# Performance work log

Measured on AMD Instinct MI355X. Metric: run time of the kernel, lower is better.

The kernel has to match this reference:

```python
import jax, jax.numpy as jnp
import numpy as np

B, CIN, T = 16, 80, 2048
C = 768          # channels
M = 512          # n_embeddings
D = 64           # z_dim
H = 256          # c_dim
N_MLP = 4        # hidden Linear(C, C) layers
LN_EPS = 1e-5
COMMIT = 0.25


def setup_inputs() -> dict:
    key = jax.random.key(0)
    ks = jax.random.split(key, 12)
    s = 0.02
    mels = jax.random.normal(ks[0], (B, CIN, T), dtype=jnp.float32)
    conv_w = jax.random.normal(ks[1], (C, CIN, 4), dtype=jnp.float32) * s  # [out, in, k]
    ln_gamma = jnp.ones((N_MLP + 1, C), dtype=jnp.float32)
    ln_beta = jnp.zeros((N_MLP + 1, C), dtype=jnp.float32)
    w_hidden = jax.random.normal(ks[2], (N_MLP, C, C), dtype=jnp.float32) * s  # [i, out, in]
    w_out = jax.random.normal(ks[3], (D, C), dtype=jnp.float32) * s
    embedding = jax.random.uniform(ks[4], (M, D), dtype=jnp.float32,
                                   minval=-1.0 / 512, maxval=1.0 / 512)
    w_ih = jax.random.normal(ks[5], (4 * H, D), dtype=jnp.float32) * s
    w_hh = jax.random.normal(ks[6], (4 * H, H), dtype=jnp.float32) * s
    b_ih = jnp.zeros((4 * H,), dtype=jnp.float32)
    b_hh = jnp.zeros((4 * H,), dtype=jnp.float32)
    return {"mels": mels, "conv_w": conv_w, "ln_gamma": ln_gamma, "ln_beta": ln_beta,
            "w_hidden": w_hidden, "w_out": w_out, "embedding": embedding,
            "w_ih": w_ih, "w_hh": w_hh, "b_ih": b_ih, "b_hh": b_hh}


def _layer_norm(x, g, b):
    mu = jnp.mean(x, axis=-1, keepdims=True)
    var = jnp.mean(jnp.square(x - mu), axis=-1, keepdims=True)
    return (x - mu) * jax.lax.rsqrt(var + LN_EPS) * g + b


def _lstm(x, w_ih, w_hh, b_ih, b_hh):
    # x: [B, T, D] -> outputs [B, T, H]; torch gate order i, f, g, o
    xg = jnp.einsum('btd,gd->btg', x, w_ih) + b_ih + b_hh  # precompute input gates

    def step(carry, xg_t):
        h, c = carry
        gates = xg_t + h @ w_hh.T
        i, f, g, o = jnp.split(gates, 4, axis=-1)
        c = jax.nn.sigmoid(f) * c + jax.nn.sigmoid(i) * jnp.tanh(g)
        h = jax.nn.sigmoid(o) * jnp.tanh(c)
        return (h, c), h

    h0 = jnp.zeros((x.shape[0], H), dtype=x.dtype)
    (_, _), hs = jax.lax.scan(step, (h0, h0), jnp.swapaxes(xg, 0, 1))
    return jnp.swapaxes(hs, 0, 1)


def reference(mels, conv_w, ln_gamma, ln_beta, w_hidden, w_out, embedding,
              w_ih, w_hh, b_ih, b_hh):
    # Conv1d(k=4, stride=2, pad=1, no bias): [B, CIN, T] -> [B, C, T//2]
    h = jax.lax.conv_general_dilated(
        mels, conv_w, window_strides=(2,), padding=[(1, 1)],
        dimension_numbers=('NCH', 'OIH', 'NCH'))
    h = jnp.swapaxes(h, 1, 2)  # [B, T', C]

    for i in range(N_MLP):
        h = jax.nn.relu(_layer_norm(h, ln_gamma[i], ln_beta[i]))
        h = h @ w_hidden[i].T
    h = jax.nn.relu(_layer_norm(h, ln_gamma[N_MLP], ln_beta[N_MLP]))
    z_beforeVQ = h @ w_out.T  # [B, T', D]

    # VQEmbeddingEMA forward (eval mode: no EMA buffer updates)
    x = z_beforeVQ
    x_flat = jax.lax.stop_gradient(x).reshape(-1, D)  # [N, D]
    dist = (jnp.sum(embedding ** 2, axis=1)[None, :]
            + jnp.sum(x_flat ** 2, axis=1, keepdims=True)
            - 2.0 * x_flat @ embedding.T)  # [N, M]
    indices = jnp.argmin(dist, axis=-1)
    quantized = embedding[indices].reshape(x.shape)
    loss = COMMIT * jnp.mean(jnp.square(x - jax.lax.stop_gradient(quantized)))
    quantized_st = x + jax.lax.stop_gradient(quantized - x)
    counts = jax.ops.segment_sum(jnp.ones_like(indices, dtype=jnp.float32),
                                 indices, num_segments=M)
    avg_probs = counts / x_flat.shape[0]
    perplexity = jnp.exp(-jnp.sum(avg_probs * jnp.log(avg_probs + 1e-10)))

    c = _lstm(quantized_st, w_ih, w_hh, b_ih, b_hh)  # [B, T', H]
    return quantized_st, c, z_beforeVQ, loss, perplexity
```

## Files before the change

### kernel.cpp

```cpp
#include <hip/hip_runtime.h>
#include <hip/hip_bf16.h>
#include <cstdint>

typedef _Float16 half2v __attribute__((ext_vector_type(2)));
typedef short bf16x8 __attribute__((ext_vector_type(8)));
typedef float f32x4v __attribute__((ext_vector_type(4)));

#define DI __device__ __forceinline__

DI half2v bch(float f)    { return __builtin_bit_cast(half2v, f); }
DI half2v bcu(unsigned u) { return __builtin_bit_cast(half2v, u); }

DI float fdot2f(half2v a, half2v b, float c) {
#if __has_builtin(__builtin_amdgcn_fdot2)
  return __builtin_amdgcn_fdot2(a, b, c, false);
#else
  return c + (float)a[0] * (float)b[0] + (float)a[1] * (float)b[1];
#endif
}

DI unsigned short bf16rne(float f) {
  unsigned u = __float_as_uint(f);
  unsigned r = (u + 0x7fffu + ((u >> 16) & 1u)) >> 16;
  return (unsigned short)r;
}
DI float bf16tof(unsigned short h) { return __uint_as_float(((unsigned)h) << 16); }

DI float blockReduceSum(float v, float* sbuf) {
  for (int off = 32; off; off >>= 1) v += __shfl_xor(v, off, 64);
  int wid = threadIdx.x >> 6;
  if ((threadIdx.x & 63) == 0) sbuf[wid] = v;
  __syncthreads();
  float r = sbuf[0] + sbuf[1] + sbuf[2] + sbuf[3];
  __syncthreads();
  return r;
}

__global__ __launch_bounds__(256) void prep_kernel(
    const float* __restrict__ conv_w, const float* __restrict__ w_hh,
    const float* __restrict__ w_ih, const float* __restrict__ b_ih,
    const float* __restrict__ b_hh, const float* __restrict__ emb,
    float* __restrict__ wT, _Float16* __restrict__ whhh,
    float* __restrict__ wihT, float* __restrict__ bias2,
    float* __restrict__ esq, int* __restrict__ counts)
{
  int idx = blockIdx.x * 256 + threadIdx.x;
  if (idx < 245760) {
    int c = idx % 768, rest = idx / 768;
    wT[idx] = conv_w[c * 320 + rest];
  }
  int i1 = idx - 245760;
  if (i1 >= 0 && i1 < 262144) whhh[i1] = (_Float16)w_hh[i1];
  int i2 = idx - (245760 + 262144);
  if (i2 >= 0 && i2 < 65536) {
    int d = i2 >> 10, grow = i2 & 1023;
    wihT[i2] = w_ih[grow * 64 + d];
  }
  int i3 = idx - (245760 + 262144 + 65536);
  if (i3 >= 0 && i3 < 1024) bias2[i3] = b_ih[i3] + b_hh[i3];
  int i4 = idx - (245760 + 262144 + 65536 + 1024);
  if (i4 >= 0 && i4 < 512) {
    float s = 0.f;
    for (int d = 0; d < 64; ++d) { float v = emb[i4 * 64 + d]; s += v * v; }
    esq[i4] = s;
  }
  int i5 = idx - (245760 + 262144 + 65536 + 1024 + 512);
  if (i5 >= 0 && i5 < 512) counts[i5] = 0;
}

__global__ __launch_bounds__(256) void wsplit_kernel(
    const float* __restrict__ w, unsigned short* __restrict__ whi,
    unsigned short* __restrict__ wlo)
{
  int idx = blockIdx.x * 256 + threadIdx.x;
  float v = w[idx];
  unsigned short h = bf16rne(v);
  whi[idx] = h;
  wlo[idx] = bf16rne(v - bf16tof(h));
}

__global__ __launch_bounds__(256) void conv_kernel(
    const float* __restrict__ mels, const float* __restrict__ wT,
    float* __restrict__ out)
{
  __shared__ float xs[80][68];
  const int bx = blockIdx.x;
  const int cblk = bx % 6;
  const int rb = bx / 6;
  const int b = rb >> 5;
  const int t0 = (rb & 31) << 5;
  const int tid = threadIdx.x;
  const int g0 = 2 * t0 - 1;
  for (int e = tid; e < 80 * 68; e += 256) {
    int ci = e / 68, ix = e % 68;
    int g = g0 + ix;
    float v = 0.f;
    if (ix < 67 && g >= 0 && g < 2048) v = mels[((size_t)b * 80 + ci) * 2048 + g];
    xs[ci][ix] = v;
  }
  __syncthreads();
  const int tc = tid & 31, tt = tid >> 5;
  const int c = cblk * 128 + tc * 4;
  float acc[4][4] = {};
  for (int ci = 0; ci < 80; ++ci) {
    float m[10];
#pragma unroll
    for (int r = 0; r < 10; ++r) m[r] = xs[ci][tt * 8 + r];
#pragma unroll
    for (int k = 0; k < 4; ++k) {
      float4 wv = *(const float4*)&wT[(size_t)(ci * 4 + k) * 768 + c];
#pragma unroll
      for (int i = 0; i < 4; ++i) {
        float mv = m[2 * i + k];
        acc[i][0] += mv * wv.x; acc[i][1] += mv * wv.y;
        acc[i][2] += mv * wv.z; acc[i][3] += mv * wv.w;
      }
    }
  }
#pragma unroll
  for (int i = 0; i < 4; ++i) {
    int tp = t0 + tt * 4 + i;
    float4 v = make_float4(acc[i][0], acc[i][1], acc[i][2], acc[i][3]);
    *(float4*)&out[((size_t)b * 1024 + tp) * 768 + c] = v;
  }
}

template<int MODE>
__global__ __launch_bounds__(256) void ln_relu_kernel(
    const float* __restrict__ in, float* __restrict__ outf,
    unsigned short* __restrict__ ohi, unsigned short* __restrict__ olo,
    const float* __restrict__ gamma, const float* __restrict__ beta)
{
  __shared__ float sbuf[4];
  const int row = blockIdx.x, tid = threadIdx.x;
  const float* p = in + (size_t)row * 768;
  float v0 = p[tid], v1 = p[tid + 256], v2 = p[tid + 512];
  float s = blockReduceSum(v0 + v1 + v2, sbuf);
  float mean = s * (1.f / 768.f);
  float d0 = v0 - mean, d1 = v1 - mean, d2 = v2 - mean;
  float sq = blockReduceSum(d0 * d0 + d1 * d1 + d2 * d2, sbuf);
  float rstd = rsqrtf(sq * (1.f / 768.f) + 1e-5f);
  float y0 = fmaxf(d0 * rstd * gamma[tid]       + beta[tid],       0.f);
  float y1 = fmaxf(d1 * rstd * gamma[tid + 256] + beta[tid + 256], 0.f);
  float y2 = fmaxf(d2 * rstd * gamma[tid + 512] + beta[tid + 512], 0.f);
  if (MODE == 0) {
    float* q = outf + (size_t)row * 768;
    q[tid] = y0; q[tid + 256] = y1; q[tid + 512] = y2;
  } else {
    unsigned short* qh = ohi + (size_t)row * 768;
    unsigned short* ql = olo + (size_t)row * 768;
    unsigned short h0 = bf16rne(y0), h1 = bf16rne(y1), h2 = bf16rne(y2);
    qh[tid] = h0; qh[tid + 256] = h1; qh[tid + 512] = h2;
    ql[tid]       = bf16rne(y0 - bf16tof(h0));
    ql[tid + 256] = bf16rne(y1 - bf16tof(h1));
    ql[tid + 512] = bf16rne(y2 - bf16tof(h2));
  }
}

__global__ __launch_bounds__(256) void mlp_gemm(
    const unsigned short* __restrict__ Ahi, const unsigned short* __restrict__ Alo,
    const unsigned short* __restrict__ Whi, const unsigned short* __restrict__ Wlo,
    float* __restrict__ C)
{
  __shared__ unsigned short As[128][40];
  __shared__ unsigned short Bs[128][40];
  const int tid = threadIdx.x;
  const int lane = tid & 63, wid = tid >> 6;
  const int wm = wid >> 1, wn = wid & 1;
  const int l15 = lane & 15, kg = lane >> 4;
  const size_t row0 = (size_t)blockIdx.y * 128;
  const int col0 = blockIdx.x * 128;
  f32x4v acc[4][4];
#pragma unroll
  for (int i = 0; i < 4; ++i)
#pragma unroll
    for (int j = 0; j < 4; ++j) acc[i][j] = (f32x4v){0.f, 0.f, 0.f, 0.f};
  for (int s = 0; s < 3; ++s) {
    const unsigned short* Ap = (s == 2) ? Alo : Ahi;
    const unsigned short* Wp = (s == 1) ? Wlo : Whi;
    for (int kt = 0; kt < 768; kt += 32) {
      __syncthreads();
#pragma unroll
      for (int it = 0; it < 2; ++it) {
        int sidx = tid + it * 256;
        int r = sidx >> 2, kc = (sidx & 3) << 3;
        uint4 va = *(const uint4*)&Ap[(row0 + r) * 768 + kt + kc];
        *(uint4*)&As[r][kc] = va;
        uint4 vb = *(const uint4*)&Wp[(size_t)(col0 + r) * 768 + kt + kc];
        *(uint4*)&Bs[r][kc] = vb;
      }
      __syncthreads();
      bf16x8 af[4], bfr[4];
#pragma unroll
      for (int mf = 0; mf < 4; ++mf)
        af[mf] = *(const bf16x8*)&As[wm * 64 + mf * 16 + l15][kg * 8];
#pragma unroll
      for (int nf = 0; nf < 4; ++nf)
        bfr[nf] = *(const bf16x8*)&Bs[wn * 64 + nf * 16 + l15][kg * 8];
#pragma unroll
      for (int mf = 0; mf < 4; ++mf)
#pragma unroll
        for (int nf = 0; nf < 4; ++nf)
          acc[mf][nf] = __builtin_amdgcn_mfma_f32_16x16x32_bf16(
              af[mf], bfr[nf], acc[mf][nf], 0, 0, 0);
    }
  }
#pragma unroll
  for (int mf = 0; mf < 4; ++mf)
#pragma unroll
    for (int nf = 0; nf < 4; ++nf)
#pragma unroll
      for (int r = 0; r < 4; ++r)
        C[(row0 + wm * 64 + mf * 16 + kg * 4 + r) * 768 +
          col0 + wn * 64 + nf * 16 + l15] = acc[mf][nf][r];
}

template<int BM, int BN, int BK, int TM, int TN>
__global__ __launch_bounds__(256) void gemm_nt(
    const float* __restrict__ A, const float* __restrict__ B,
    float* __restrict__ C, int M, int N, int K)
{
  constexpr int LDA = BM + 4, LDB = BN + 4;
  __shared__ float As[BK][LDA];
  __shared__ float Bs[BK][LDB];
  const int tid = threadIdx.x;
  const size_t row0 = (size_t)blockIdx.y * BM;
  const size_t col0 = (size_t)blockIdx.x * BN;
  const int tx = tid & 15, ty = tid >> 4;
  constexpr int GSM = BM * 4 / TM;
  constexpr int GSN = BN * 4 / TN;
  constexpr int F4R = BK / 4;
  constexpr int AIT = BM * BK / 4 / 256;
  constexpr int BIT = BN * BK / 4 / 256;
  static_assert(AIT * 256 * 4 == BM * BK, "A tile divisibility");
  static_assert(BIT * 256 * 4 == BN * BK, "B tile divisibility");
  float acc[TM][TN] = {};
  for (int kt = 0; kt < K; kt += BK) {
#pragma unroll
    for (int p = 0; p < AIT; ++p) {
      int item = tid + p * 256;
      int r = item / F4R, q = item % F4R;
      float4 v = *(const float4*)&A[(row0 + r) * K + kt + q * 4];
      As[q * 4 + 0][r] = v.x; As[q * 4 + 1][r] = v.y;
      As[q * 4 + 2][r] = v.z; As[q * 4 + 3][r] = v.w;
    }
#pragma unroll
    for (int p = 0; p < BIT; ++p) {
      int item = tid + p * 256;
      int r = item / F4R, q = item % F4R;
      float4 v = *(const float4*)&B[(col0 + r) * K + kt + q * 4];
      Bs[q * 4 + 0][r] = v.x; Bs[q * 4 + 1][r] = v.y;
      Bs[q * 4 + 2][r] = v.z; Bs[q * 4 + 3][r] = v.w;
    }
    __syncthreads();
#pragma unroll
    for (int k = 0; k < BK; ++k) {
      float a[TM], b[TN];
#pragma unroll
      for (int g = 0; g < TM / 4; ++g) {
        float4 v = *(const float4*)&As[k][ty * 4 + g * GSM];
        a[g * 4 + 0] = v.x; a[g * 4 + 1] = v.y; a[g * 4 + 2] = v.z; a[g * 4 + 3] = v.w;
      }
#pragma unroll
      for (int g = 0; g < TN / 4; ++g) {
        float4 v = *(const float4*)&Bs[k][tx * 4 + g * GSN];
        b[g * 4 + 0] = v.x; b[g * 4 + 1] = v.y; b[g * 4 + 2] = v.z; b[g * 4 + 3] = v.w;
      }
#pragma unroll
      for (int i = 0; i < TM; ++i)
#pragma unroll
        for (int j = 0; j < TN; ++j)
          acc[i][j] += a[i] * b[j];
    }
    __syncthreads();
  }
#pragma unroll
  for (int i = 0; i < TM; ++i) {
    size_t row = row0 + ty * 4 + (i >> 2) * GSM + (i & 3);
#pragma unroll
    for (int g = 0; g < TN / 4; ++g) {
      float4 v = make_float4(acc[i][g * 4 + 0], acc[i][g * 4 + 1],
                             acc[i][g * 4 + 2], acc[i][g * 4 + 3]);
      *(float4*)&C[row * N + col0 + tx * 4 + g * GSN] = v;
    }
  }
}

DI unsigned int ordbits(float f) {
  unsigned int u = __float_as_uint(f);
  return (u & 0x80000000u) ? ~u : (u | 0x80000000u);
}

__global__ __launch_bounds__(128) void vq_argmin_kernel(
    const float* __restrict__ dots, const float* __restrict__ esq,
    const float* __restrict__ emb, const float* __restrict__ z,
    float* __restrict__ quant, int* __restrict__ counts,
    float* __restrict__ lossrow)
{
  __shared__ unsigned long long sred[2];
  const int row = blockIdx.x, tid = threadIdx.x;
  float4 d4 = *(const float4*)&dots[(size_t)row * 512 + tid * 4];
  float4 e4 = *(const float4*)&esq[tid * 4];
  float dist[4] = { e4.x - 2.f * d4.x, e4.y - 2.f * d4.y,
                    e4.z - 2.f * d4.z, e4.w - 2.f * d4.w };
  unsigned long long best =
      ((unsigned long long)ordbits(dist[0]) << 32) | (unsigned)(tid * 4);
#pragma unroll
  for (int c2 = 1; c2 < 4; ++c2) {
    unsigned long long k =
        ((unsigned long long)ordbits(dist[c2]) << 32) | (unsigned)(tid * 4 + c2);
    best = (k < best) ? k : best;
  }
  for (int off = 32; off; off >>= 1) {
    unsigned long long o = __shfl_xor(best, off, 64);
    best = (o < best) ? o : best;
  }
  if ((tid & 63) == 0) sred[tid >> 6] = best;
  __syncthreads();
  unsigned long long fin = sred[0] < sred[1] ? sred[0] : sred[1];
  int bi = (int)(fin & 0xffffffffu);
  if (tid < 64) {
    float e = emb[(size_t)bi * 64 + tid];
    quant[(size_t)row * 64 + tid] = e;
    float df = z[(size_t)row * 64 + tid] - e;
    float s = df * df;
    for (int off = 32; off; off >>= 1) s += __shfl_xor(s, off, 64);
    if (tid == 0) {
      lossrow[row] = s;
      atomicAdd(&counts[bi], 1);
    }
  }
}

__global__ __launch_bounds__(256) void finalize_kernel(
    const float* __restrict__ lossrow, const int* __restrict__ counts,
    float* __restrict__ loss_out, float* __restrict__ perp_out)
{
  __shared__ float sbuf[4];
  const int tid = threadIdx.x;
  float s = 0.f;
  for (int i = tid; i < 16384; i += 256) s += lossrow[i];
  s = blockReduceSum(s, sbuf);
  float t = 0.f;
  for (int e = tid; e < 512; e += 256) {
    float p = (float)counts[e] * (1.f / 16384.f);
    t += p * logf(p + 1e-10f);
  }
  t = blockReduceSum(t, sbuf);
  if (tid == 0) {
    *loss_out = 0.25f * s / (16384.f * 64.f);
    *perp_out = expf(-t);
  }
}

__global__ __launch_bounds__(256) void xg_kernel(
    const float* __restrict__ q, const float* __restrict__ wihT,
    const float* __restrict__ bias2, float* __restrict__ xg3)
{
  __shared__ float qs[8][64];
  const int r0 = blockIdx.x * 8, tid = threadIdx.x;
  for (int e = tid; e < 512; e += 256)
    qs[e >> 6][e & 63] = q[(size_t)r0 * 64 + e];
  __syncthreads();
  float4 bias = *(const float4*)&bias2[tid * 4];
  float4 acc[8];
#pragma unroll
  for (int r = 0; r < 8; ++r) acc[r] = bias;
  for (int d = 0; d < 64; ++d) {
    float4 wv = *(const float4*)&wihT[d * 1024 + tid * 4];
#pragma unroll
    for (int r = 0; r < 8; ++r) {
      float qv = qs[r][d];
      acc[r].x += qv * wv.x; acc[r].y += qv * wv.y;
      acc[r].z += qv * wv.z; acc[r].w += qv * wv.w;
    }
  }
#pragma unroll
  for (int r = 0; r < 8; ++r)
    *(float4*)&xg3[(size_t)(r0 + r) * 1024 + tid * 4] = acc[r];
}

#define W24(M) M(0) M(1) M(2) M(3) M(4) M(5) M(6) M(7) M(8) M(9) M(10) M(11) \
               M(12) M(13) M(14) M(15) M(16) M(17) M(18) M(19) M(20) M(21) M(22) M(23)
#define DECLW(J) uint4 wa##J = pA[J]; uint4 wb##J = pB[J];
#define DOTR(J) { float4 h4 = hb4[J]; \
  a0 = fdot2f(bcu(wa##J.x), bch(h4.x), a0); b0 = fdot2f(bcu(wb##J.x), bch(h4.x), b0); \
  a1 = fdot2f(bcu(wa##J.y), bch(h4.y), a1); b1 = fdot2f(bcu(wb##J.y), bch(h4.y), b1); \
  a0 = fdot2f(bcu(wa##J.z), bch(h4.z), a0); b0 = fdot2f(bcu(wb##J.z), bch(h4.z), b0); \
  a1 = fdot2f(bcu(wa##J.w), bch(h4.w), a1); b1 = fdot2f(bcu(wb##J.w), bch(h4.w), b1); }

__global__ __launch_bounds__(512, 2) void lstm_kernel(
    const float* __restrict__ xg3, const _Float16* __restrict__ whhh,
    float* __restrict__ cout)
{
  __shared__ unsigned wlds[1024 * 36];
  __shared__ __align__(16) _Float16 hb[256];
  __shared__ float gbuf[512];
  const int tid = threadIdx.x;
  const int b = blockIdx.x;
  const int jloc = tid & 255;
  const int half = tid >> 8;
  const int rA = half * 256 + jloc;
  const int rB = 512 + half * 256 + jloc;
  {
    const unsigned* wsrc = (const unsigned*)whhh;
    for (int idx = tid; idx < 1024 * 32; idx += 512) {
      int row = idx >> 5, kp = idx & 31;
      wlds[row * 36 + kp] = wsrc[row * 128 + 96 + kp];
    }
  }
  if (tid < 256) hb[tid] = (_Float16)0.f;
  const uint4* pA = (const uint4*)(whhh + (size_t)rA * 256);
  const uint4* pB = (const uint4*)(whhh + (size_t)rB * 256);
  W24(DECLW)
  const size_t bT = (size_t)b * 1024;
  const int rA36 = rA * 36, rB36 = rB * 36;
  float cst = 0.f;
  float xgA = xg3[bT * 1024 + rA];
  float xgB = xg3[bT * 1024 + rB];
  __syncthreads();
  for (int t = 0; t < 1024; ++t) {
    float nxA = 0.f, nxB = 0.f;
    if (t < 1023) {
      nxA = xg3[(bT + t + 1) * 1024 + rA];
      nxB = xg3[(bT + t + 1) * 1024 + rB];
    }
    float a0 = 0.f, a1 = 0.f, b0 = 0.f, b1 = 0.f;
    const float4* hb4 = (const float4*)hb;
    W24(DOTR)
#pragma unroll
    for (int j = 0; j < 8; ++j) {
      float4 h4 = hb4[24 + j];
      uint4 wa = *(const uint4*)&wlds[rA36 + 4 * j];
      uint4 wb = *(const uint4*)&wlds[rB36 + 4 * j];
      a0 = fdot2f(bcu(wa.x), bch(h4.x), a0); b0 = fdot2f(bcu(wb.x), bch(h4.x), b0);
      a1 = fdot2f(bcu(wa.y), bch(h4.y), a1); b1 = fdot2f(bcu(wb.y), bch(h4.y), b1);
      a0 = fdot2f(bcu(wa.z), bch(h4.z), a0); b0 = fdot2f(bcu(wb.z), bch(h4.z), b0);
      a1 = fdot2f(bcu(wa.w), bch(h4.w), a1); b1 = fdot2f(bcu(wb.w), bch(h4.w), b1);
    }
    float gA = a0 + a1 + xgA;
    float gB = b0 + b1 + xgB;
    if (half) { gbuf[jloc] = gA; gbuf[256 + jloc] = gB; }
    __syncthreads();
    if (!half) {
      float gf = gbuf[jloc], go = gbuf[256 + jloc];
      float si = 1.f / (1.f + __expf(-gA));
      float sf = 1.f / (1.f + __expf(-gf));
      float so = 1.f / (1.f + __expf(-go));
      float tg = 1.f - 2.f / (1.f + __expf(2.f * gB));
      cst = sf * cst + si * tg;
      float tc = 1.f - 2.f / (1.f + __expf(2.f * cst));
      float h = so * tc;
      cout[(bT + t) * 256 + jloc] = h;
      hb[jloc] = (_Float16)h;
    }
    __syncthreads();
    xgA = nxA; xgB = nxB;
  }
}

extern "C" void kernel_launch(void* const* d_in, const int* in_sizes, int n_in,
                              void* d_out, int out_size, void* d_ws, size_t ws_size,
                              hipStream_t stream)
{
  const float* mels   = (const float*)d_in[0];
  const float* conv_w = (const float*)d_in[1];
  const float* ln_g   = (const float*)d_in[2];
  const float* ln_b   = (const float*)d_in[3];
  const float* w_hid  = (const float*)d_in[4];
  const float* w_out  = (const float*)d_in[5];
  const float* emb    = (const float*)d_in[6];
  const float* w_ih   = (const float*)d_in[7];
  const float* w_hh   = (const float*)d_in[8];
  const float* b_ih   = (const float*)d_in[9];
  const float* b_hh   = (const float*)d_in[10];

  float* out = (float*)d_out;
  float* q_out   = out;
  float* c_out   = out + 1048576;
  float* z_out   = out + 5242880;
  float* loss_out = out + 6291456;
  float* perp_out = out + 6291457;

  char* ws = (char*)d_ws;
  float*  hA    = (float*)(ws + 0);
  float*  hB    = (float*)(ws + 50331648);
  unsigned short* Ahi = (unsigned short*)(ws + 50331648);
  unsigned short* Alo = (unsigned short*)(ws + 75497472);
  float*  dots  = (float*)(ws + 0);
  float*  xg3   = (float*)(ws + 50331648);
  char* wsw = ws + 117440512;
  float*    wT     = (float*)(wsw);
  _Float16* whhh   = (_Float16*)(wsw + 983040);
  float*    wihT   = (float*)(wsw + 1507328);
  float*    bias2  = (float*)(wsw + 1769472);
  float*    esq    = (float*)(wsw + 1773568);
  int*      counts = (int*)  (wsw + 1775616);
  float*    lossrow= (float*)(wsw + 1777664);
  unsigned short* Whi = (unsigned short*)((char*)d_out + 4194304);
  unsigned short* Wlo = Whi + 2359296;
  if (ws_size < 119283712u) return;

  prep_kernel<<<2248, 256, 0, stream>>>(conv_w, w_hh, w_ih, b_ih, b_hh, emb,
                                        wT, whhh, wihT, bias2, esq, counts);
  wsplit_kernel<<<9216, 256, 0, stream>>>(w_hid, Whi, Wlo);
  conv_kernel<<<3072, 256, 0, stream>>>(mels, wT, hA);
  for (int l = 0; l < 4; ++l) {
    ln_relu_kernel<1><<<16384, 256, 0, stream>>>(
        hA, nullptr, Ahi, Alo, ln_g + l * 768, ln_b + l * 768);
    mlp_gemm<<<dim3(6, 128), 256, 0, stream>>>(
        Ahi, Alo, Whi + (size_t)l * 589824, Wlo + (size_t)l * 589824, hA);
  }
  ln_relu_kernel<0><<<16384, 256, 0, stream>>>(
      hA, hB, nullptr, nullptr, ln_g + 4 * 768, ln_b + 4 * 768);
  gemm_nt<128, 64, 16, 8, 4><<<dim3(1, 128), 256, 0, stream>>>(
      hB, w_out, z_out, 16384, 64, 768);
  gemm_nt<128, 128, 16, 8, 8><<<dim3(4, 128), 256, 0, stream>>>(
      z_out, emb, dots, 16384, 512, 64);
  vq_argmin_kernel<<<16384, 128, 0, stream>>>(dots, esq, emb, z_out,
                                              q_out, counts, lossrow);
  finalize_kernel<<<1, 256, 0, stream>>>(lossrow, counts, loss_out, perp_out);
  xg_kernel<<<2048, 256, 0, stream>>>(q_out, wihT, bias2, xg3);
  lstm_kernel<<<16, 512, 0, stream>>>(xg3, whhh, c_out);
}
```

Before: 2.664 ms.

## Use 1024 threads per LSTM block, one gate row per thread

The LSTM recurrence kernel now launches 1024 threads per batch block, so each thread computes one gate row instead of two. Each thread keeps 23 of its row's 32 fp16 weight chunks in registers and reads the other 9 from LDS, which is now filled with 36 words per row. All gate preactivations go through shared memory before the 256 cell-update threads run. The aim is a shorter serial dot product per time step. In exchange the block has half the registers per thread and more threads wait at each barrier.

```diff
diff --git a/kernel.cpp b/kernel.cpp
--- a/kernel.cpp
+++ b/kernel.cpp
@@ -380,82 +380,71 @@
     *(float4*)&xg3[(size_t)(r0 + r) * 1024 + tid * 4] = acc[r];
 }
 
-#define W24(M) M(0) M(1) M(2) M(3) M(4) M(5) M(6) M(7) M(8) M(9) M(10) M(11) \
-               M(12) M(13) M(14) M(15) M(16) M(17) M(18) M(19) M(20) M(21) M(22) M(23)
-#define DECLW(J) uint4 wa##J = pA[J]; uint4 wb##J = pB[J];
+#define W23(M) M(0) M(1) M(2) M(3) M(4) M(5) M(6) M(7) M(8) M(9) M(10) M(11) \
+               M(12) M(13) M(14) M(15) M(16) M(17) M(18) M(19) M(20) M(21) M(22)
+#define DECLW(J) uint4 w##J = pA[J];
 #define DOTR(J) { float4 h4 = hb4[J]; \
-  a0 = fdot2f(bcu(wa##J.x), bch(h4.x), a0); b0 = fdot2f(bcu(wb##J.x), bch(h4.x), b0); \
-  a1 = fdot2f(bcu(wa##J.y), bch(h4.y), a1); b1 = fdot2f(bcu(wb##J.y), bch(h4.y), b1); \
-  a0 = fdot2f(bcu(wa##J.z), bch(h4.z), a0); b0 = fdot2f(bcu(wb##J.z), bch(h4.z), b0); \
-  a1 = fdot2f(bcu(wa##J.w), bch(h4.w), a1); b1 = fdot2f(bcu(wb##J.w), bch(h4.w), b1); }
-
-__global__ __launch_bounds__(512, 2) void lstm_kernel(
+  a0 = fdot2f(bcu(w##J.x), bch(h4.x), a0); \
+  a1 = fdot2f(bcu(w##J.y), bch(h4.y), a1); \
+  a0 = fdot2f(bcu(w##J.z), bch(h4.z), a0); \
+  a1 = fdot2f(bcu(w##J.w), bch(h4.w), a1); }
+
+__global__ __launch_bounds__(1024) void lstm_kernel(
     const float* __restrict__ xg3, const _Float16* __restrict__ whhh,
     float* __restrict__ cout)
 {
   __shared__ unsigned wlds[1024 * 36];
   __shared__ __align__(16) _Float16 hb[256];
-  __shared__ float gbuf[512];
+  __shared__ float gbuf[1024];
   const int tid = threadIdx.x;
   const int b = blockIdx.x;
-  const int jloc = tid & 255;
-  const int half = tid >> 8;
-  const int rA = half * 256 + jloc;
-  const int rB = 512 + half * 256 + jloc;
   {
     const unsigned* wsrc = (const unsigned*)whhh;
-    for (int idx = tid; idx < 1024 * 32; idx += 512) {
-      int row = idx >> 5, kp = idx & 31;
-      wlds[row * 36 + kp] = wsrc[row * 128 + 96 + kp];
+    for (int idx = tid; idx < 1024 * 36; idx += 1024) {
+      int row = idx / 36, kp = idx - row * 36;
+      wlds[row * 36 + kp] = wsrc[row * 128 + 92 + kp];
     }
   }
   if (tid < 256) hb[tid] = (_Float16)0.f;
-  const uint4* pA = (const uint4*)(whhh + (size_t)rA * 256);
-  const uint4* pB = (const uint4*)(whhh + (size_t)rB * 256);
-  W24(DECLW)
+  const uint4* pA = (const uint4*)(whhh + (size_t)tid * 256);
+  W23(DECLW)
   const size_t bT = (size_t)b * 1024;
-  const int rA36 = rA * 36, rB36 = rB * 36;
+  const int r36 = tid * 36;
   float cst = 0.f;
-  float xgA = xg3[bT * 1024 + rA];
-  float xgB = xg3[bT * 1024 + rB];
+  float xgv = xg3[bT * 1024 + tid];
   __syncthreads();
   for (int t = 0; t < 1024; ++t) {
-    float nxA = 0.f, nxB = 0.f;
-    if (t < 1023) {
-      nxA = xg3[(bT + t + 1) * 1024 + rA];
-      nxB = xg3[(bT + t + 1) * 1024 + rB];
-    }
-    float a0 = 0.f, a1 = 0.f, b0 = 0.f, b1 = 0.f;
+    float nx = 0.f;
+    if (t < 1023) nx = xg3[(bT + t + 1) * 1024 + tid];
+    float a0 = 0.f, a1 = 0.f;
     const float4* hb4 = (const float4*)hb;
-    W24(DOTR)
-#pragma unroll
-    for (int j = 0; j < 8; ++j) {
-      float4 h4 = hb4[24 + j];
-      uint4 wa = *(const uint4*)&wlds[rA36 + 4 * j];
-      uint4 wb = *(const uint4*)&wlds[rB36 + 4 * j];
-      a0 = fdot2f(bcu(wa.x), bch(h4.x), a0); b0 = fdot2f(bcu(wb.x), bch(h4.x), b0);
-      a1 = fdot2f(bcu(wa.y), bch(h4.y), a1); b1 = fdot2f(bcu(wb.y), bch(h4.y), b1);
-      a0 = fdot2f(bcu(wa.z), bch(h4.z), a0); b0 = fdot2f(bcu(wb.z), bch(h4.z), b0);
-      a1 = fdot2f(bcu(wa.w), bch(h4.w), a1); b1 = fdot2f(bcu(wb.w), bch(h4.w), b1);
-    }
-    float gA = a0 + a1 + xgA;
-    float gB = b0 + b1 + xgB;
-    if (half) { gbuf[jloc] = gA; gbuf[256 + jloc] = gB; }
+    W23(DOTR)
+#pragma unroll
+    for (int jj = 0; jj < 9; ++jj) {
+      float4 h4 = hb4[23 + jj];
+      uint4 wl = *(const uint4*)&wlds[r36 + 4 * jj];
+      a0 = fdot2f(bcu(wl.x), bch(h4.x), a0);
+      a1 = fdot2f(bcu(wl.y), bch(h4.y), a1);
+      a0 = fdot2f(bcu(wl.z), bch(h4.z), a0);
+      a1 = fdot2f(bcu(wl.w), bch(h4.w), a1);
+    }
+    gbuf[tid] = a0 + a1 + xgv;
     __syncthreads();
-    if (!half) {
-      float gf = gbuf[jloc], go = gbuf[256 + jloc];
-      float si = 1.f / (1.f + __expf(-gA));
+    if (tid < 256) {
+      float gi = gbuf[tid], gf = gbuf[256 + tid],
+            gg = gbuf[512 + tid], go = gbuf[768 + tid];
+      float si = 1.f / (1.f + __expf(-gi));
       float sf = 1.f / (1.f + __expf(-gf));
       float so = 1.f / (1.f + __expf(-go));
-      float tg = 1.f - 2.f / (1.f + __expf(2.f * gB));
+      float tg = 1.f - 2.f / (1.f + __expf(2.f * gg));
       cst = sf * cst + si * tg;
       float tc = 1.f - 2.f / (1.f + __expf(2.f * cst));
       float h = so * tc;
-      cout[(bT + t) * 256 + jloc] = h;
-      hb[jloc] = (_Float16)h;
+      cout[(bT + t) * 256 + tid] = h;
+      hb[tid] = (_Float16)h;
     }
     __syncthreads();
-    xgA = nxA; xgB = nxB;
+    xgv = nx;
   }
 }
 
@@ -521,5 +510,5 @@
                                               q_out, counts, lossrow);
   finalize_kernel<<<1, 256, 0, stream>>>(lossrow, counts, loss_out, perp_out);
   xg_kernel<<<2048, 256, 0, stream>>>(q_out, wihT, bias2, xg3);
-  lstm_kernel<<<16, 512, 0, stream>>>(xg3, whhh, c_out);
-}
+  lstm_kernel<<<16, 1024, 0, stream>>>(xg3, whhh, c_out);
+}
```

New measurement: 2.866 ms. +7.6%, slower.
